# Performance work log

Measured on AMD Instinct MI355X. Metric: run time of the kernel, lower is better.

Reference implementation:

```python
import jax, jax.numpy as jnp
import numpy as np

N = 50000
E = 1000000
WIDTH = 64
DEPTH = 4


def setup_inputs() -> dict:
    key = jax.random.key(0)
    ks = jax.random.split(key, 6)
    x = jax.random.normal(ks[0], (N, 5), dtype=jnp.float32)
    edge_index = jax.random.randint(ks[1], (2, E), 0, N, dtype=jnp.int32)
    edge_attr = jax.random.normal(ks[2], (E, 3), dtype=jnp.float32)
    w1 = jax.random.normal(ks[3], (3, WIDTH), dtype=jnp.float32) / jnp.sqrt(3.0)
    b1 = jnp.zeros((WIDTH,), jnp.float32)
    w2 = jax.random.normal(ks[4], (WIDTH, 1), dtype=jnp.float32) / jnp.sqrt(float(WIDTH))
    b2 = jnp.zeros((1,), jnp.float32)
    root = jax.random.normal(ks[5], (1, 1), dtype=jnp.float32)
    bias = jnp.zeros((1,), jnp.float32)
    return dict(x=x, edge_index=edge_index, edge_attr=edge_attr,
                w1=w1, b1=b1, w2=w2, b2=b2, root=root, bias=bias)


def reference(x, edge_index, edge_attr, w1, b1, w2, b2, root, bias):
    # h: scalar node feature, column 2 of data.x -> [N, 1]
    h = x[:, 2:3]
    src, dst = edge_index[0], edge_index[1]  # messages flow src -> dst

    # Per-edge 1x1 weight from the edge MLP (depends only on edge_attr,
    # identical for all depth iterations since the conv is shared).
    w_e = jax.nn.relu(edge_attr @ w1 + b1) @ w2 + b2  # [E, 1]

    # Mean aggregation: precompute in-degree of each target node.
    deg = jax.ops.segment_sum(jnp.ones((E,), jnp.float32), dst, num_segments=N)
    inv_deg = jnp.where(deg > 0, 1.0 / jnp.maximum(deg, 1.0), 0.0)[:, None]  # [N, 1]

    for _ in range(DEPTH):
        msg = h[src] * w_e                                        # gather + per-edge weight, [E, 1]
        agg = jax.ops.segment_sum(msg, dst, num_segments=N) * inv_deg  # scatter-mean, [N, 1]
        h = jax.nn.relu(agg + h @ root + bias)                    # root transform + bias + ReLU
    return h
```

## Files before the change

### kernel.cpp

```cpp
#include <hip/hip_runtime.h>

#define NN 50000
#define NNP 50176
#define NE 1000000
#define NBK 196
#define EPB 1024
#define PB 977
#define ESTRIDE 5632

__global__ void init_fixed(const float* __restrict__ x, float* __restrict__ hA,
                           int* __restrict__ cursor, int* __restrict__ sBeg,
                           int* __restrict__ sLim) {
    int i = blockIdx.x * 256 + threadIdx.x;
    if (i < NN) hA[i] = x[5 * i + 2];
    if (i < NBK) {
        cursor[i] = i * ESTRIDE;
        sBeg[i]   = i * ESTRIDE;
        sLim[i]   = (i + 1) * ESTRIDE;
    }
}

__global__ void place_kernel(const float* __restrict__ ea,
                             const int* __restrict__ src,
                             const int* __restrict__ dst,
                             const float* __restrict__ w1,
                             const float* __restrict__ b1,
                             const float* __restrict__ w2,
                             const float* __restrict__ b2,
                             const int* __restrict__ sLim,
                             int* __restrict__ cursor,
                             uint2* __restrict__ es,
                             int dumpbase) {
    __shared__ float sw1[192];
    __shared__ float sb1[64];
    __shared__ float sw2[64];
    __shared__ float sce[EPB];
    __shared__ int hist[NBK];
    __shared__ int hbase[NBK];
    int t = threadIdx.x;
    if (t < 192) sw1[t] = w1[t];
    if (t < 64) { sb1[t] = b1[t]; sw2[t] = w2[t]; }
    if (t < NBK) hist[t] = 0;
    __syncthreads();

    int r[4], dd[4];
#pragma unroll
    for (int j = 0; j < 4; ++j) {
        int e = blockIdx.x * EPB + j * 256 + t;
        dd[j] = -1;
        if (e < NE) {
            float a0 = ea[3 * e + 0];
            float a1 = ea[3 * e + 1];
            float a2 = ea[3 * e + 2];
            float c0 = b2[0], c1 = 0.f, c2 = 0.f, c3 = 0.f;
#pragma unroll
            for (int k = 0; k < 64; k += 4) {
                float h0 = fmaf(a0, sw1[k+0], fmaf(a1, sw1[64+k+0], fmaf(a2, sw1[128+k+0], sb1[k+0])));
                float h1 = fmaf(a0, sw1[k+1], fmaf(a1, sw1[64+k+1], fmaf(a2, sw1[128+k+1], sb1[k+1])));
                float h2 = fmaf(a0, sw1[k+2], fmaf(a1, sw1[64+k+2], fmaf(a2, sw1[128+k+2], sb1[k+2])));
                float h3 = fmaf(a0, sw1[k+3], fmaf(a1, sw1[64+k+3], fmaf(a2, sw1[128+k+3], sb1[k+3])));
                c0 = fmaf(fmaxf(h0, 0.f), sw2[k+0], c0);
                c1 = fmaf(fmaxf(h1, 0.f), sw2[k+1], c1);
                c2 = fmaf(fmaxf(h2, 0.f), sw2[k+2], c2);
                c3 = fmaf(fmaxf(h3, 0.f), sw2[k+3], c3);
            }
            sce[j * 256 + t] = (c0 + c1) + (c2 + c3);
            int d = dst[e];
            dd[j] = d;
            r[j] = atomicAdd(&hist[d >> 8], 1);
        }
    }
    __syncthreads();
    if (t < NBK) { int hv = hist[t]; if (hv) hbase[t] = atomicAdd(&cursor[t], hv); }
    __syncthreads();
#pragma unroll
    for (int j = 0; j < 4; ++j) {
        int e = blockIdx.x * EPB + j * 256 + t;
        if (e < NE) {
            int d = dd[j];
            int b = d >> 8;
            int pos = hbase[b] + r[j];
            if (pos >= sLim[b]) pos = dumpbase + (t & 63);
            unsigned pack = (unsigned)src[e] | ((unsigned)(d & 255) << 17);
            es[pos] = make_uint2(pack, __float_as_uint(sce[j * 256 + t]));
        }
    }
}

__global__ __launch_bounds__(1024)
void reorder_kernel(const int* __restrict__ cursor,
                    const uint2* __restrict__ es,
                    uint2* __restrict__ es2,
                    int* __restrict__ pEnd) {
    __shared__ int hist[256];
    __shared__ int part[256];
    __shared__ int cur[NBK];
    int t = threadIdx.x;
    int b = blockIdx.x;
    if (t < 256) hist[t] = 0;
    __syncthreads();
    int s0 = b * ESTRIDE;
    int cap = s0 + ESTRIDE;
    int s1 = cursor[b];
    if (s1 > cap) s1 = cap;

    uint2 v[6]; int sg[6]; bool mv[6];
#pragma unroll
    for (int k = 0; k < 6; ++k) {
        int p = s0 + k * 1024 + t;
        mv[k] = (p < s1);
        if (mv[k]) {
            v[k] = es[p];
            sg[k] = (v[k].x >> 8) & 0x1FF;
            atomicAdd(&hist[sg[k]], 1);
        }
    }
    __syncthreads();
    int val = 0;
    if (t < 256) { val = hist[t]; part[t] = val; }
    __syncthreads();
    for (int off = 1; off < 256; off <<= 1) {
        int xv = 0, add = 0;
        if (t < 256) { xv = part[t]; if (t >= off) add = part[t - off]; }
        __syncthreads();
        if (t < 256) part[t] = xv + add;
        __syncthreads();
    }
    if (t < NBK) cur[t] = s0 + part[t] - val;
    __syncthreads();
#pragma unroll
    for (int k = 0; k < 6; ++k) {
        if (mv[k]) {
            int pos = atomicAdd(&cur[sg[k]], 1);
            if (pos >= cap) pos = NBK * ESTRIDE + (t & 63);
            unsigned pk = (v[k].x & 255u) | (((v[k].x >> 17) & 255u) << 8);
            es2[pos] = make_uint2(pk, v[k].y);
        }
    }
    __syncthreads();
    if (t < NBK) pEnd[b * NBK + t] = cur[t];
}

template<int FIRST>
__global__ __launch_bounds__(1024)
void round2(const int* __restrict__ pEnd,
            const uint2* __restrict__ es2,
            const float* __restrict__ hold,
            float* __restrict__ hnew,
            float* __restrict__ invdeg,
            const float* __restrict__ root,
            const float* __restrict__ bias) {
    __shared__ float sh[16][256];
    __shared__ float lagg[256];
    __shared__ int ldeg[256];
    int t = threadIdx.x;
    int b = blockIdx.x;
    int lane = t & 63, w = t >> 6;
    float ho = 0.f;
    int node = b * 256 + t;
    if (t < 256) {
        lagg[t] = 0.f;
        if (FIRST) ldeg[t] = 0;
        if (node < NN) ho = hold[node];
    }
    __syncthreads();

    const float4* h4 = (const float4*)hold;
    const int pb = b * NBK;
    const int base0 = b * ESTRIDE;
    const int cap = base0 + ESTRIDE;
    float* shw = &sh[w][0];

    int s = w;
    float4 hv = h4[s * 64 + lane];
    int beg = (s == 0) ? base0 : pEnd[pb + s - 1];
    int end = pEnd[pb + s];
    if (beg > cap) beg = cap;
    if (end > cap) end = cap;
    uint2 ev; bool evm = (beg + lane < end);
    if (evm) ev = es2[beg + lane];

    while (s < NBK) {
        int ns = s + 16;
        float4 nhv; int nbeg = 0, nend = 0; uint2 nev; bool nevm = false;
        if (ns < NBK) {
            nhv = h4[ns * 64 + lane];
            nbeg = pEnd[pb + ns - 1];
            nend = pEnd[pb + ns];
            if (nbeg > cap) nbeg = cap;
            if (nend > cap) nend = cap;
            nevm = (nbeg + lane < nend);
            if (nevm) nev = es2[nbeg + lane];
        }
        shw[lane * 4 + 0] = hv.x;
        shw[lane * 4 + 1] = hv.y;
        shw[lane * 4 + 2] = hv.z;
        shw[lane * 4 + 3] = hv.w;
        if (evm) {
            float hs = shw[ev.x & 255];
            int dl = (ev.x >> 8) & 255;
            atomicAdd(&lagg[dl], hs * __uint_as_float(ev.y));
            if (FIRST) atomicAdd(&ldeg[dl], 1);
        }
        for (int p = beg + lane + 64; p < end; p += 64) {
            uint2 vv = es2[p];
            float hs = shw[vv.x & 255];
            int dl = (vv.x >> 8) & 255;
            atomicAdd(&lagg[dl], hs * __uint_as_float(vv.y));
            if (FIRST) atomicAdd(&ldeg[dl], 1);
        }
        s = ns; hv = nhv; beg = nbeg; end = nend; ev = nev; evm = nevm;
    }
    __syncthreads();

    if (t < 256 && node < NN) {
        float inv;
        if (FIRST) {
            int d = ldeg[t];
            inv = (d > 0) ? (1.0f / (float)d) : 0.f;
            invdeg[node] = inv;
        } else {
            inv = invdeg[node];
        }
        hnew[node] = fmaxf(fmaf(ho, root[0], fmaf(lagg[t], inv, bias[0])), 0.f);
    }
}

__global__ void bucket_count(const int* __restrict__ dst, int* __restrict__ bcnt,
                             const float* __restrict__ x, float* __restrict__ h) {
    __shared__ int hist[NBK];
    int t = threadIdx.x;
    if (t < NBK) hist[t] = 0;
    __syncthreads();
    int gid = blockIdx.x * 256 + t;
    if (gid < NN) h[gid] = x[5 * gid + 2];
#pragma unroll
    for (int j = 0; j < 4; ++j) {
        int e = blockIdx.x * EPB + j * 256 + t;
        if (e < NE) atomicAdd(&hist[dst[e] >> 8], 1);
    }
    __syncthreads();
    if (t < NBK && hist[t]) atomicAdd(&bcnt[t], hist[t]);
}

__global__ void bucket_scan(const int* __restrict__ bcnt,
                            int* __restrict__ sBeg,
                            int* __restrict__ cursor,
                            int* __restrict__ sLim) {
    __shared__ int part[256];
    int t = threadIdx.x;
    int v = (t < NBK) ? ((bcnt[t] + 1) & ~1) : 0;
    part[t] = v;
    __syncthreads();
    for (int off = 1; off < 256; off <<= 1) {
        int x = part[t];
        int add = (t >= off) ? part[t - off] : 0;
        __syncthreads();
        part[t] = x + add;
        __syncthreads();
    }
    if (t < NBK) {
        int excl = part[t] - v;
        sBeg[t] = excl;
        cursor[t] = excl;
        sLim[t] = 0x7FFFFFFF;
    }
}

template<int FIRST>
__global__ __launch_bounds__(1024)
void round_fused(const int* __restrict__ sBeg,
                 const int* __restrict__ sEnd,
                 const int* __restrict__ sLim,
                 const uint2* __restrict__ es,
                 const float* __restrict__ hold,
                 float* __restrict__ hnew,
                 float* __restrict__ invdeg,
                 const float* __restrict__ root,
                 const float* __restrict__ bias) {
    __shared__ float lagg[256];
    __shared__ int ldeg[256];
    int t = threadIdx.x;
    int b = blockIdx.x;
    if (t < 256) { lagg[t] = 0.f; if (FIRST) ldeg[t] = 0; }
    __syncthreads();
    int s0 = sBeg[b];
    int s1 = sEnd[b];
    { int cap = sLim[b]; if (s1 > cap) s1 = cap; }
    const uint4* es4 = (const uint4*)es;
    for (int p = s0 + t * 2; p < s1; p += 2048) {
        uint4 v = es4[p >> 1];
        {
            int sidx = v.x & 0x1FFFF;
            int dl = (v.x >> 17) & 255;
            atomicAdd(&lagg[dl], hold[sidx] * __uint_as_float(v.y));
            if (FIRST) atomicAdd(&ldeg[dl], 1);
        }
        if (p + 1 < s1) {
            int sidx = v.z & 0x1FFFF;
            int dl = (v.z >> 17) & 255;
            atomicAdd(&lagg[dl], hold[sidx] * __uint_as_float(v.w));
            if (FIRST) atomicAdd(&ldeg[dl], 1);
        }
    }
    __syncthreads();
    if (t < 256) {
        int node = b * 256 + t;
        if (node < NN) {
            float inv;
            if (FIRST) {
                int d = ldeg[t];
                inv = (d > 0) ? (1.0f / (float)d) : 0.f;
                invdeg[node] = inv;
            } else {
                inv = invdeg[node];
            }
            hnew[node] = fmaxf(fmaf(hold[node], root[0], fmaf(lagg[t], inv, bias[0])), 0.f);
        }
    }
}


extern "C" void kernel_launch(void* const* d_in, const int* in_sizes, int n_in,
                              void* d_out, int out_size, void* d_ws, size_t ws_size,
                              hipStream_t stream) {
    const float* x    = (const float*)d_in[0];
    const int*   ei   = (const int*)d_in[1];
    const float* ea   = (const float*)d_in[2];
    const float* w1   = (const float*)d_in[3];
    const float* b1   = (const float*)d_in[4];
    const float* w2   = (const float*)d_in[5];
    const float* b2   = (const float*)d_in[6];
    const float* root = (const float*)d_in[7];
    const float* bias = (const float*)d_in[8];

    const int* src = ei;
    const int* dst = ei + NE;
    float* out = (float*)d_out;

    const int BLK = 256;
    const int gN = (NN + BLK - 1) / BLK;

    const size_t esN = (size_t)NBK * ESTRIDE + 64;
    const size_t needFixed = esN * 8 * 2
                           + (size_t)(NBK * NBK) * 4
                           + (size_t)(NBK * 3) * 4
                           + (size_t)NNP * 4 * 3;

    if (ws_size >= needFixed) {
        uint2* es     = (uint2*)d_ws;
        uint2* es2    = es + esN;
        int*   pEnd   = (int*)(es2 + esN);
        int*   cursor = pEnd + NBK * NBK;
        int*   sBeg   = cursor + NBK;
        int*   sLim   = sBeg + NBK;
        float* invdeg = (float*)(sLim + NBK);
        float* hA     = invdeg + NNP;
        float* hB     = hA + NNP;

        init_fixed<<<NBK, BLK, 0, stream>>>(x, hA, cursor, sBeg, sLim);
        place_kernel<<<PB, BLK, 0, stream>>>(ea, src, dst, w1, b1, w2, b2,
                                             sLim, cursor, es, (int)(NBK * ESTRIDE));
        reorder_kernel<<<NBK, 1024, 0, stream>>>(cursor, es, es2, pEnd);
        round2<1><<<NBK, 1024, 0, stream>>>(pEnd, es2, hA, hB, invdeg, root, bias);
        round2<0><<<NBK, 1024, 0, stream>>>(pEnd, es2, hB, hA, invdeg, root, bias);
        round2<0><<<NBK, 1024, 0, stream>>>(pEnd, es2, hA, hB, invdeg, root, bias);
        round2<0><<<NBK, 1024, 0, stream>>>(pEnd, es2, hB, out, invdeg, root, bias);
    } else {
        uint2* es     = (uint2*)d_ws;
        int*   bcnt   = (int*)(es + NE + NBK);
        int*   cursor = bcnt + NBK;
        int*   sBeg   = cursor + NBK;
        int*   sLim   = sBeg + NBK;
        float* invdeg = (float*)(sLim + NBK);
        float* hB     = invdeg + NN;
        float* h      = out;

        hipMemsetAsync(bcnt, 0, NBK * 4, stream);
        bucket_count<<<PB, BLK, 0, stream>>>(dst, bcnt, x, h);
        bucket_scan<<<1, 256, 0, stream>>>(bcnt, sBeg, cursor, sLim);
        place_kernel<<<PB, BLK, 0, stream>>>(ea, src, dst, w1, b1, w2, b2,
                                             sLim, cursor, es, 0);
        round_fused<1><<<NBK, 1024, 0, stream>>>(sBeg, cursor, sLim, es, h,  hB, invdeg, root, bias);
        round_fused<0><<<NBK, 1024, 0, stream>>>(sBeg, cursor, sLim, es, hB, h,  invdeg, root, bias);
        round_fused<0><<<NBK, 1024, 0, stream>>>(sBeg, cursor, sLim, es, h,  hB, invdeg, root, bias);
        round_fused<0><<<NBK, 1024, 0, stream>>>(sBeg, cursor, sLim, es, hB, h,  invdeg, root, bias);
    }
}
```

Baseline: 167.4 us.

## Replace global atomic bucketing with per-block segment slots and fuse reorder into first round

The edge placement kernel now writes each edge into a fixed per-(bucket, block) slot region of capacity 64 using only shared-memory counters. This removes the init kernel and the global cursor atomics. The separate reorder kernel is folded into the first round, which sorts edges by source sub-bucket in LDS and writes the compacted list once. Later rounds stage the bucket's edges into LDS before aggregating. The risks are silent overflow when a segment exceeds 64 or a bucket exceeds ESTRIDE, a larger sparse slot array to scan, and heavy LDS use that limits occupancy.

Measured after the change: 415.9 us. +148.4%, slower.

```diff
diff --git a/kernel.cpp b/kernel.cpp
--- a/kernel.cpp
+++ b/kernel.cpp
@@ -4,19 +4,244 @@
 #define NNP 50176
 #define NE 1000000
 #define NBK 196
+#define ESTRIDE 5632
+#define SEGCAP 64
+#define BSTRIDE (NBK * SEGCAP)
+#define EPB2 5120
+
 #define EPB 1024
 #define PB 977
-#define ESTRIDE 5632
-
-__global__ void init_fixed(const float* __restrict__ x, float* __restrict__ hA,
-                           int* __restrict__ cursor, int* __restrict__ sBeg,
-                           int* __restrict__ sLim) {
-    int i = blockIdx.x * 256 + threadIdx.x;
-    if (i < NN) hA[i] = x[5 * i + 2];
-    if (i < NBK) {
-        cursor[i] = i * ESTRIDE;
-        sBeg[i]   = i * ESTRIDE;
-        sLim[i]   = (i + 1) * ESTRIDE;
+
+__global__ __launch_bounds__(1024)
+void place2(const float* __restrict__ x,
+            const float* __restrict__ ea,
+            const int* __restrict__ src,
+            const int* __restrict__ dst,
+            const float* __restrict__ w1,
+            const float* __restrict__ b1,
+            const float* __restrict__ w2,
+            const float* __restrict__ b2,
+            uint2* __restrict__ es,
+            int* __restrict__ cnt,
+            float* __restrict__ hA) {
+    __shared__ float sw1[192];
+    __shared__ float sb1[64];
+    __shared__ float sw2[64];
+    __shared__ int hist[NBK];
+    const int t = threadIdx.x;
+    const int j = blockIdx.x;
+    if (t < 192) sw1[t] = w1[t];
+    if (t < 64) { sb1[t] = b1[t]; sw2[t] = w2[t]; }
+    if (t < NBK) hist[t] = 0;
+    {
+        int i = j * 1024 + t;
+        if (i < NN) hA[i] = x[5 * i + 2];
+    }
+    __syncthreads();
+    const float bz = b2[0];
+
+    for (int k = 0; k < 5; ++k) {
+        int e = j * EPB2 + k * 1024 + t;
+        if (e < NE) {
+            float a0 = ea[3 * e + 0];
+            float a1 = ea[3 * e + 1];
+            float a2 = ea[3 * e + 2];
+            float c0 = bz, c1 = 0.f, c2 = 0.f, c3 = 0.f;
+#pragma unroll
+            for (int kk = 0; kk < 64; kk += 4) {
+                float h0 = fmaf(a0, sw1[kk+0], fmaf(a1, sw1[64+kk+0], fmaf(a2, sw1[128+kk+0], sb1[kk+0])));
+                float h1 = fmaf(a0, sw1[kk+1], fmaf(a1, sw1[64+kk+1], fmaf(a2, sw1[128+kk+1], sb1[kk+1])));
+                float h2 = fmaf(a0, sw1[kk+2], fmaf(a1, sw1[64+kk+2], fmaf(a2, sw1[128+kk+2], sb1[kk+2])));
+                float h3 = fmaf(a0, sw1[kk+3], fmaf(a1, sw1[64+kk+3], fmaf(a2, sw1[128+kk+3], sb1[kk+3])));
+                c0 = fmaf(fmaxf(h0, 0.f), sw2[kk+0], c0);
+                c1 = fmaf(fmaxf(h1, 0.f), sw2[kk+1], c1);
+                c2 = fmaf(fmaxf(h2, 0.f), sw2[kk+2], c2);
+                c3 = fmaf(fmaxf(h3, 0.f), sw2[kk+3], c3);
+            }
+            float ce = (c0 + c1) + (c2 + c3);
+            int d = dst[e];
+            int b = d >> 8;
+            int r = atomicAdd(&hist[b], 1);
+            int pos = (r < SEGCAP) ? (b * BSTRIDE + j * SEGCAP + r)
+                                   : (NBK * BSTRIDE + (t & 63));
+            es[pos] = make_uint2((unsigned)src[e] | ((unsigned)(d & 255) << 17),
+                                 __float_as_uint(ce));
+        }
+    }
+    __syncthreads();
+    if (t < NBK) { int hv = hist[t]; cnt[j * NBK + t] = (hv > SEGCAP) ? SEGCAP : hv; }
+}
+
+template<int FIRST>
+__global__ __launch_bounds__(1024)
+void roundK(const int* __restrict__ cnt,
+            const uint2* __restrict__ es,
+            uint2* __restrict__ es2,
+            int* __restrict__ pEnd,
+            const float* __restrict__ hold,
+            float* __restrict__ hnew,
+            float* __restrict__ invdeg,
+            const float* __restrict__ root,
+            const float* __restrict__ bias) {
+    __shared__ uint2 eLDS[ESTRIDE];
+    __shared__ float sh[16][256];
+    __shared__ int hist[256];
+    __shared__ int part[256];
+    __shared__ int scanE[256];
+    __shared__ int cur[NBK];
+    __shared__ int cnt_l[NBK];
+    __shared__ float lagg[256];
+    __shared__ int ldeg[256];
+    const int t = threadIdx.x;
+    const int b = blockIdx.x;
+    const int lane = t & 63, w = t >> 6;
+    const int node = b * 256 + t;
+    const int base0 = b * ESTRIDE;
+    float ho = 0.f;
+    if (t < 256) {
+        lagg[t] = 0.f;
+        if (FIRST) ldeg[t] = 0;
+        if (node < NN) ho = hold[node];
+    }
+
+    if (FIRST) {
+        if (t < 256) hist[t] = 0;
+        if (t < NBK) cnt_l[t] = cnt[t * NBK + b];
+        __syncthreads();
+        for (int s0 = 0; s0 < NBK * SEGCAP; s0 += 1024) {
+            int s = s0 + t;
+            if (s < NBK * SEGCAP) {
+                int jj = s >> 6, idx = s & 63;
+                if (idx < cnt_l[jj]) {
+                    uint2 v = es[b * BSTRIDE + s];
+                    atomicAdd(&hist[(v.x >> 8) & 0x1FF], 1);
+                }
+            }
+        }
+        __syncthreads();
+        int val = 0;
+        if (t < 256) { val = hist[t]; part[t] = val; }
+        __syncthreads();
+        for (int off = 1; off < 256; off <<= 1) {
+            int xv = 0, add = 0;
+            if (t < 256) { xv = part[t]; if (t >= off) add = part[t - off]; }
+            __syncthreads();
+            if (t < 256) part[t] = xv + add;
+            __syncthreads();
+        }
+        if (t < 256) scanE[t] = (part[t] < ESTRIDE) ? part[t] : ESTRIDE;
+        if (t < NBK) cur[t] = part[t] - val;
+        if (t < NBK) pEnd[b * NBK + t] = base0 + ((part[t] < ESTRIDE) ? part[t] : ESTRIDE);
+        __syncthreads();
+        for (int s0 = 0; s0 < NBK * SEGCAP; s0 += 1024) {
+            int s = s0 + t;
+            if (s < NBK * SEGCAP) {
+                int jj = s >> 6, idx = s & 63;
+                if (idx < cnt_l[jj]) {
+                    uint2 v = es[b * BSTRIDE + s];
+                    int sg = (v.x >> 8) & 0x1FF;
+                    int pos = atomicAdd(&cur[sg], 1);
+                    if (pos < ESTRIDE)
+                        eLDS[pos] = make_uint2((v.x & 255u) | (((v.x >> 17) & 255u) << 8), v.y);
+                }
+            }
+        }
+        __syncthreads();
+        {
+            int total = scanE[NBK - 1];
+            for (int p = t; p < total; p += 1024) es2[base0 + p] = eLDS[p];
+        }
+    } else {
+        if (t < NBK) {
+            int e0 = pEnd[b * NBK + t] - base0;
+            scanE[t] = (e0 < ESTRIDE) ? e0 : ESTRIDE;
+        }
+        __syncthreads();
+        int total = scanE[NBK - 1];
+        for (int p = t; p < total; p += 1024) eLDS[p] = es2[base0 + p];
+        __syncthreads();
+    }
+
+    float* shw = &sh[w][0];
+    const float4* h4 = (const float4*)hold;
+    int s = w;
+    float4 hv = h4[s * 64 + lane];
+    int beg = (s == 0) ? 0 : scanE[s - 1];
+    int end = scanE[s];
+    while (s < NBK) {
+        int ns = s + 16;
+        float4 nhv; int nbeg = 0, nend = 0;
+        if (ns < NBK) {
+            nhv = h4[ns * 64 + lane];
+            nbeg = scanE[ns - 1];
+            nend = scanE[ns];
+        }
+        shw[lane * 4 + 0] = hv.x;
+        shw[lane * 4 + 1] = hv.y;
+        shw[lane * 4 + 2] = hv.z;
+        shw[lane * 4 + 3] = hv.w;
+        for (int p = beg + lane; p < end; p += 64) {
+            uint2 vv = eLDS[p];
+            float hs = shw[vv.x & 255];
+            int dl = (vv.x >> 8) & 255;
+            atomicAdd(&lagg[dl], hs * __uint_as_float(vv.y));
+            if (FIRST) atomicAdd(&ldeg[dl], 1);
+        }
+        s = ns; hv = nhv; beg = nbeg; end = nend;
+    }
+    __syncthreads();
+
+    if (t < 256 && node < NN) {
+        float inv;
+        if (FIRST) {
+            int d = ldeg[t];
+            inv = (d > 0) ? (1.0f / (float)d) : 0.f;
+            invdeg[node] = inv;
+        } else {
+            inv = invdeg[node];
+        }
+        hnew[node] = fmaxf(fmaf(ho, root[0], fmaf(lagg[t], inv, bias[0])), 0.f);
+    }
+}
+
+__global__ void bucket_count(const int* __restrict__ dst, int* __restrict__ bcnt,
+                             const float* __restrict__ x, float* __restrict__ h) {
+    __shared__ int hist[NBK];
+    int t = threadIdx.x;
+    if (t < NBK) hist[t] = 0;
+    __syncthreads();
+    int gid = blockIdx.x * 256 + t;
+    if (gid < NN) h[gid] = x[5 * gid + 2];
+#pragma unroll
+    for (int j = 0; j < 4; ++j) {
+        int e = blockIdx.x * EPB + j * 256 + t;
+        if (e < NE) atomicAdd(&hist[dst[e] >> 8], 1);
+    }
+    __syncthreads();
+    if (t < NBK && hist[t]) atomicAdd(&bcnt[t], hist[t]);
+}
+
+__global__ void bucket_scan(const int* __restrict__ bcnt,
+                            int* __restrict__ sBeg,
+                            int* __restrict__ cursor,
+                            int* __restrict__ sLim) {
+    __shared__ int part[256];
+    int t = threadIdx.x;
+    int v = (t < NBK) ? ((bcnt[t] + 1) & ~1) : 0;
+    part[t] = v;
+    __syncthreads();
+    for (int off = 1; off < 256; off <<= 1) {
+        int x = part[t];
+        int add = (t >= off) ? part[t - off] : 0;
+        __syncthreads();
+        part[t] = x + add;
+        __syncthreads();
+    }
+    if (t < NBK) {
+        int excl = part[t] - v;
+        sBeg[t] = excl;
+        cursor[t] = excl;
+        sLim[t] = 0x7FFFFFFF;
     }
 }
 
@@ -87,186 +312,6 @@
     }
 }
 
-__global__ __launch_bounds__(1024)
-void reorder_kernel(const int* __restrict__ cursor,
-                    const uint2* __restrict__ es,
-                    uint2* __restrict__ es2,
-                    int* __restrict__ pEnd) {
-    __shared__ int hist[256];
-    __shared__ int part[256];
-    __shared__ int cur[NBK];
-    int t = threadIdx.x;
-    int b = blockIdx.x;
-    if (t < 256) hist[t] = 0;
-    __syncthreads();
-    int s0 = b * ESTRIDE;
-    int cap = s0 + ESTRIDE;
-    int s1 = cursor[b];
-    if (s1 > cap) s1 = cap;
-
-    uint2 v[6]; int sg[6]; bool mv[6];
-#pragma unroll
-    for (int k = 0; k < 6; ++k) {
-        int p = s0 + k * 1024 + t;
-        mv[k] = (p < s1);
-        if (mv[k]) {
-            v[k] = es[p];
-            sg[k] = (v[k].x >> 8) & 0x1FF;
-            atomicAdd(&hist[sg[k]], 1);
-        }
-    }
-    __syncthreads();
-    int val = 0;
-    if (t < 256) { val = hist[t]; part[t] = val; }
-    __syncthreads();
-    for (int off = 1; off < 256; off <<= 1) {
-        int xv = 0, add = 0;
-        if (t < 256) { xv = part[t]; if (t >= off) add = part[t - off]; }
-        __syncthreads();
-        if (t < 256) part[t] = xv + add;
-        __syncthreads();
-    }
-    if (t < NBK) cur[t] = s0 + part[t] - val;
-    __syncthreads();
-#pragma unroll
-    for (int k = 0; k < 6; ++k) {
-        if (mv[k]) {
-            int pos = atomicAdd(&cur[sg[k]], 1);
-            if (pos >= cap) pos = NBK * ESTRIDE + (t & 63);
-            unsigned pk = (v[k].x & 255u) | (((v[k].x >> 17) & 255u) << 8);
-            es2[pos] = make_uint2(pk, v[k].y);
-        }
-    }
-    __syncthreads();
-    if (t < NBK) pEnd[b * NBK + t] = cur[t];
-}
-
-template<int FIRST>
-__global__ __launch_bounds__(1024)
-void round2(const int* __restrict__ pEnd,
-            const uint2* __restrict__ es2,
-            const float* __restrict__ hold,
-            float* __restrict__ hnew,
-            float* __restrict__ invdeg,
-            const float* __restrict__ root,
-            const float* __restrict__ bias) {
-    __shared__ float sh[16][256];
-    __shared__ float lagg[256];
-    __shared__ int ldeg[256];
-    int t = threadIdx.x;
-    int b = blockIdx.x;
-    int lane = t & 63, w = t >> 6;
-    float ho = 0.f;
-    int node = b * 256 + t;
-    if (t < 256) {
-        lagg[t] = 0.f;
-        if (FIRST) ldeg[t] = 0;
-        if (node < NN) ho = hold[node];
-    }
-    __syncthreads();
-
-    const float4* h4 = (const float4*)hold;
-    const int pb = b * NBK;
-    const int base0 = b * ESTRIDE;
-    const int cap = base0 + ESTRIDE;
-    float* shw = &sh[w][0];
-
-    int s = w;
-    float4 hv = h4[s * 64 + lane];
-    int beg = (s == 0) ? base0 : pEnd[pb + s - 1];
-    int end = pEnd[pb + s];
-    if (beg > cap) beg = cap;
-    if (end > cap) end = cap;
-    uint2 ev; bool evm = (beg + lane < end);
-    if (evm) ev = es2[beg + lane];
-
-    while (s < NBK) {
-        int ns = s + 16;
-        float4 nhv; int nbeg = 0, nend = 0; uint2 nev; bool nevm = false;
-        if (ns < NBK) {
-            nhv = h4[ns * 64 + lane];
-            nbeg = pEnd[pb + ns - 1];
-            nend = pEnd[pb + ns];
-            if (nbeg > cap) nbeg = cap;
-            if (nend > cap) nend = cap;
-            nevm = (nbeg + lane < nend);
-            if (nevm) nev = es2[nbeg + lane];
-        }
-        shw[lane * 4 + 0] = hv.x;
-        shw[lane * 4 + 1] = hv.y;
-        shw[lane * 4 + 2] = hv.z;
-        shw[lane * 4 + 3] = hv.w;
-        if (evm) {
-            float hs = shw[ev.x & 255];
-            int dl = (ev.x >> 8) & 255;
-            atomicAdd(&lagg[dl], hs * __uint_as_float(ev.y));
-            if (FIRST) atomicAdd(&ldeg[dl], 1);
-        }
-        for (int p = beg + lane + 64; p < end; p += 64) {
-            uint2 vv = es2[p];
-            float hs = shw[vv.x & 255];
-            int dl = (vv.x >> 8) & 255;
-            atomicAdd(&lagg[dl], hs * __uint_as_float(vv.y));
-            if (FIRST) atomicAdd(&ldeg[dl], 1);
-        }
-        s = ns; hv = nhv; beg = nbeg; end = nend; ev = nev; evm = nevm;
-    }
-    __syncthreads();
-
-    if (t < 256 && node < NN) {
-        float inv;
-        if (FIRST) {
-            int d = ldeg[t];
-            inv = (d > 0) ? (1.0f / (float)d) : 0.f;
-            invdeg[node] = inv;
-        } else {
-            inv = invdeg[node];
-        }
-        hnew[node] = fmaxf(fmaf(ho, root[0], fmaf(lagg[t], inv, bias[0])), 0.f);
-    }
-}
-
-__global__ void bucket_count(const int* __restrict__ dst, int* __restrict__ bcnt,
-                             const float* __restrict__ x, float* __restrict__ h) {
-    __shared__ int hist[NBK];
-    int t = threadIdx.x;
-    if (t < NBK) hist[t] = 0;
-    __syncthreads();
-    int gid = blockIdx.x * 256 + t;
-    if (gid < NN) h[gid] = x[5 * gid + 2];
-#pragma unroll
-    for (int j = 0; j < 4; ++j) {
-        int e = blockIdx.x * EPB + j * 256 + t;
-        if (e < NE) atomicAdd(&hist[dst[e] >> 8], 1);
-    }
-    __syncthreads();
-    if (t < NBK && hist[t]) atomicAdd(&bcnt[t], hist[t]);
-}
-
-__global__ void bucket_scan(const int* __restrict__ bcnt,
-                            int* __restrict__ sBeg,
-                            int* __restrict__ cursor,
-                            int* __restrict__ sLim) {
-    __shared__ int part[256];
-    int t = threadIdx.x;
-    int v = (t < NBK) ? ((bcnt[t] + 1) & ~1) : 0;
-    part[t] = v;
-    __syncthreads();
-    for (int off = 1; off < 256; off <<= 1) {
-        int x = part[t];
-        int add = (t >= off) ? part[t - off] : 0;
-        __syncthreads();
-        part[t] = x + add;
-        __syncthreads();
-    }
-    if (t < NBK) {
-        int excl = part[t] - v;
-        sBeg[t] = excl;
-        cursor[t] = excl;
-        sLim[t] = 0x7FFFFFFF;
-    }
-}
-
 template<int FIRST>
 __global__ __launch_bounds__(1024)
 void round_fused(const int* __restrict__ sBeg,
@@ -338,34 +383,26 @@
     const int* dst = ei + NE;
     float* out = (float*)d_out;
 
-    const int BLK = 256;
-    const int gN = (NN + BLK - 1) / BLK;
-
-    const size_t esN = (size_t)NBK * ESTRIDE + 64;
-    const size_t needFixed = esN * 8 * 2
-                           + (size_t)(NBK * NBK) * 4
-                           + (size_t)(NBK * 3) * 4
+    const size_t esSlots = (size_t)NBK * BSTRIDE + 64;
+    const size_t es2N    = (size_t)NBK * ESTRIDE;
+    const size_t needFixed = esSlots * 8 + es2N * 8
+                           + (size_t)(NBK * NBK) * 4 * 2
                            + (size_t)NNP * 4 * 3;
 
     if (ws_size >= needFixed) {
         uint2* es     = (uint2*)d_ws;
-        uint2* es2    = es + esN;
-        int*   pEnd   = (int*)(es2 + esN);
-        int*   cursor = pEnd + NBK * NBK;
-        int*   sBeg   = cursor + NBK;
-        int*   sLim   = sBeg + NBK;
-        float* invdeg = (float*)(sLim + NBK);
+        uint2* es2    = es + esSlots;
+        int*   cnt    = (int*)(es2 + es2N);
+        int*   pEnd   = cnt + NBK * NBK;
+        float* invdeg = (float*)(pEnd + NBK * NBK);
         float* hA     = invdeg + NNP;
         float* hB     = hA + NNP;
 
-        init_fixed<<<NBK, BLK, 0, stream>>>(x, hA, cursor, sBeg, sLim);
-        place_kernel<<<PB, BLK, 0, stream>>>(ea, src, dst, w1, b1, w2, b2,
-                                             sLim, cursor, es, (int)(NBK * ESTRIDE));
-        reorder_kernel<<<NBK, 1024, 0, stream>>>(cursor, es, es2, pEnd);
-        round2<1><<<NBK, 1024, 0, stream>>>(pEnd, es2, hA, hB, invdeg, root, bias);
-        round2<0><<<NBK, 1024, 0, stream>>>(pEnd, es2, hB, hA, invdeg, root, bias);
-        round2<0><<<NBK, 1024, 0, stream>>>(pEnd, es2, hA, hB, invdeg, root, bias);
-        round2<0><<<NBK, 1024, 0, stream>>>(pEnd, es2, hB, out, invdeg, root, bias);
+        place2<<<NBK, 1024, 0, stream>>>(x, ea, src, dst, w1, b1, w2, b2, es, cnt, hA);
+        roundK<1><<<NBK, 1024, 0, stream>>>(cnt, es, es2, pEnd, hA, hB, invdeg, root, bias);
+        roundK<0><<<NBK, 1024, 0, stream>>>(cnt, es, es2, pEnd, hB, hA, invdeg, root, bias);
+        roundK<0><<<NBK, 1024, 0, stream>>>(cnt, es, es2, pEnd, hA, hB, invdeg, root, bias);
+        roundK<0><<<NBK, 1024, 0, stream>>>(cnt, es, es2, pEnd, hB, out, invdeg, root, bias);
     } else {
         uint2* es     = (uint2*)d_ws;
         int*   bcnt   = (int*)(es + NE + NBK);
@@ -377,9 +414,9 @@
         float* h      = out;
 
         hipMemsetAsync(bcnt, 0, NBK * 4, stream);
-        bucket_count<<<PB, BLK, 0, stream>>>(dst, bcnt, x, h);
+        bucket_count<<<PB, 256, 0, stream>>>(dst, bcnt, x, h);
         bucket_scan<<<1, 256, 0, stream>>>(bcnt, sBeg, cursor, sLim);
-        place_kernel<<<PB, BLK, 0, stream>>>(ea, src, dst, w1, b1, w2, b2,
+        place_kernel<<<PB, 256, 0, stream>>>(ea, src, dst, w1, b1, w2, b2,
                                              sLim, cursor, es, 0);
         round_fused<1><<<NBK, 1024, 0, stream>>>(sBeg, cursor, sLim, es, h,  hB, invdeg, root, bias);
         round_fused<0><<<NBK, 1024, 0, stream>>>(sBeg, cursor, sLim, es, hB, h,  invdeg, root, bias);
```
